# Performance work log

Measured on AMD Instinct MI355X. Metric: run time of the kernel, lower is better.

## Reference

```python
import jax, jax.numpy as jnp
import numpy as np

B, NQ = 4, 4096
HF, WF = 96, 96          # single-level feature map -> Nv = 9216
NV = HF * WF
E = 768                  # dim * num_frames = 192 * 4
NH, NP, NL = 8, 4, 1
HD = E // NH             # 96
EPS = 1e-6


def _layer_norm(x, w, b):
    m = jnp.mean(x, axis=-1, keepdims=True)
    v = jnp.var(x, axis=-1, keepdims=True)
    return (x - m) * jax.lax.rsqrt(v + EPS) * w + b


def _msda_core(value, shapes, loc, aw):
    # value: (B, Nv, H, D); loc: (B, Nq, H, L, P, 2) normalized in [0,1];
    # aw: (B, Nq, H, L, P). Bilinear sampling matching F.grid_sample
    # (align_corners=False, padding_mode='zeros'): pixel = loc * size - 0.5.
    Bn, Nv, H, D = value.shape
    Nq, P = loc.shape[1], loc.shape[4]
    out = jnp.zeros((Bn, H, Nq, D), value.dtype)
    start = 0
    for lvl in range(shapes.shape[0]):
        Hl, Wl = int(shapes[lvl, 0]), int(shapes[lvl, 1])
        v = value[:, start:start + Hl * Wl].transpose(0, 2, 1, 3)  # (B,H,S,D)
        start += Hl * Wl
        x = loc[:, :, :, lvl, :, 0] * Wl - 0.5  # (B,Nq,H,P)
        y = loc[:, :, :, lvl, :, 1] * Hl - 0.5
        x0, y0 = jnp.floor(x), jnp.floor(y)
        sampled = jnp.zeros((Bn, H, Nq, P, D), value.dtype)
        for dx in (0, 1):
            for dy in (0, 1):
                xi, yi = x0 + dx, y0 + dy
                w = (1.0 - jnp.abs(x - xi)) * (1.0 - jnp.abs(y - yi))
                valid = (xi >= 0) & (xi <= Wl - 1) & (yi >= 0) & (yi <= Hl - 1)
                idx = (jnp.clip(yi, 0, Hl - 1) * Wl
                       + jnp.clip(xi, 0, Wl - 1)).astype(jnp.int32)
                idx = idx.transpose(0, 2, 1, 3).reshape(Bn, H, Nq * P)
                g = jnp.take_along_axis(v, idx[..., None], axis=2)
                g = g.reshape(Bn, H, Nq, P, D)
                wz = jnp.where(valid, w, 0.0).transpose(0, 2, 1, 3)[..., None]
                sampled = sampled + g * wz
        awl = aw[:, :, :, lvl].transpose(0, 2, 1, 3)[..., None]  # (B,H,Nq,P,1)
        out = out + jnp.sum(sampled * awl, axis=3)
    return out.transpose(0, 2, 1, 3).reshape(Bn, Nq, H * D)


def setup_inputs():
    key = jax.random.key(0)
    ks = jax.random.split(key, 12)
    s = 0.02
    return {
        "query": jax.random.normal(ks[0], (B, NQ, E), jnp.float32),
        "reference_points": jax.random.uniform(ks[1], (B, NQ, NL, 2), jnp.float32),
        "feat": jax.random.normal(ks[2], (B, NV, E), jnp.float32),
        "spatial_shapes": jnp.array([[HF, WF]], jnp.int32),
        "level_start_index": jnp.zeros((NL,), jnp.int32),
        "ln_q_w": jnp.ones((E,), jnp.float32),
        "ln_q_b": jnp.zeros((E,), jnp.float32),
        "ln_f_w": jnp.ones((E,), jnp.float32),
        "ln_f_b": jnp.zeros((E,), jnp.float32),
        "W_value": jax.random.normal(ks[3], (E, E), jnp.float32) * s,
        "b_value": jnp.zeros((E,), jnp.float32),
        "W_off": jax.random.normal(ks[4], (E, NH * NL * NP * 2), jnp.float32) * s,
        "b_off": jax.random.normal(ks[5], (NH * NL * NP * 2,), jnp.float32) * s,
        "W_attn": jax.random.normal(ks[6], (E, NH * NL * NP), jnp.float32) * s,
        "b_attn": jnp.zeros((NH * NL * NP,), jnp.float32),
        "W_out": jax.random.normal(ks[7], (E, E), jnp.float32) * s,
        "b_out": jnp.zeros((E,), jnp.float32),
        "gamma": jax.random.normal(ks[8], (E,), jnp.float32) * s,
    }


def reference(query, reference_points, feat, spatial_shapes, level_start_index,
              ln_q_w, ln_q_b, ln_f_w, ln_f_b, W_value, b_value, W_off, b_off,
              W_attn, b_attn, W_out, b_out, gamma):
    shapes = np.asarray(spatial_shapes)  # static level shapes
    Bn, Nq, _ = query.shape
    Nv = feat.shape[1]
    q = _layer_norm(query, ln_q_w, ln_q_b)
    f = _layer_norm(feat, ln_f_w, ln_f_b)
    value = (f @ W_value + b_value).reshape(Bn, Nv, NH, HD)
    offsets = (q @ W_off + b_off).reshape(Bn, Nq, NH, NL, NP, 2)
    aw = jax.nn.softmax((q @ W_attn + b_attn).reshape(Bn, Nq, NH, NL * NP), -1)
    aw = aw.reshape(Bn, Nq, NH, NL, NP)
    # offset_normalizer = [W_l, H_l] per level
    norm = jnp.stack([jnp.asarray(shapes[:, 1], jnp.float32),
                      jnp.asarray(shapes[:, 0], jnp.float32)], axis=-1)  # (L,2)
    loc = (reference_points[:, :, None, :, None, :]
           + offsets / norm[None, None, None, :, None, :])
    out = _msda_core(value, shapes, loc, aw)
    out = out @ W_out + b_out
    attn = q + out  # mmcv MSDeformAttn adds identity (dropout=eval no-op)
    return query + gamma * attn
```

## Files before the change

kernel.cpp:

```cpp
#include <hip/hip_runtime.h>

#define BB     4
#define NQS    4096
#define NVS    9216
#define E_DIM  768
#define NHEAD  8
#define NPTS   4
#define HDIM   96
#define HFEAT  96
#define WFEAT  96
#define MQR    16384

typedef __attribute__((ext_vector_type(8))) short  s8v;
typedef __attribute__((ext_vector_type(4))) short  s4v;
typedef __attribute__((ext_vector_type(4))) float  f4v;

__device__ __forceinline__ unsigned short f2bf(float x) {
    unsigned int u = __builtin_bit_cast(unsigned int, x);
    unsigned int r = (u + 0x7fffu + ((u >> 16) & 1u)) >> 16;
    return (unsigned short)r;
}
__device__ __forceinline__ float bf2f(unsigned short s) {
    unsigned int u = ((unsigned int)s) << 16;
    return __builtin_bit_cast(float, u);
}
__device__ __forceinline__ float bf2f_s(short s) {
    return bf2f((unsigned short)s);
}

#define GLD16(gp, lp) \
    __builtin_amdgcn_global_load_lds( \
        (__attribute__((address_space(1))) void*)(gp), \
        (__attribute__((address_space(3))) void*)(lp), 16, 0, 0)

__global__ __launch_bounds__(256) void ln_fused_kernel(
    const float* __restrict__ q, const float* __restrict__ f,
    const float* __restrict__ qw, const float* __restrict__ qb,
    const float* __restrict__ fw, const float* __restrict__ fb,
    unsigned short* __restrict__ qout, unsigned short* __restrict__ fout,
    float* __restrict__ stats) {
    const int wv = threadIdx.x >> 6, lane = threadIdx.x & 63;
    const int row = blockIdx.x * 4 + wv;
    const bool isq = row < MQR;
    const float* x = isq ? (q + (size_t)row * E_DIM)
                         : (f + (size_t)(row - MQR) * E_DIM);
    const float4 v0 = ((const float4*)x)[lane];
    const float4 v1 = ((const float4*)x)[lane + 64];
    const float4 v2 = ((const float4*)x)[lane + 128];
    float s1 = v0.x + v0.y + v0.z + v0.w + v1.x + v1.y + v1.z + v1.w
             + v2.x + v2.y + v2.z + v2.w;
    float s2 = v0.x * v0.x + v0.y * v0.y + v0.z * v0.z + v0.w * v0.w
             + v1.x * v1.x + v1.y * v1.y + v1.z * v1.z + v1.w * v1.w
             + v2.x * v2.x + v2.y * v2.y + v2.z * v2.z + v2.w * v2.w;
    #pragma unroll
    for (int o = 32; o > 0; o >>= 1) {
        s1 += __shfl_down(s1, o, 64);
        s2 += __shfl_down(s2, o, 64);
    }
    const float mean = __shfl(s1, 0, 64) * (1.0f / E_DIM);
    const float m2   = __shfl(s2, 0, 64) * (1.0f / E_DIM);
    const float rstd = rsqrtf(m2 - mean * mean + 1e-6f);
    if (isq && lane == 0) { stats[row * 2] = mean; stats[row * 2 + 1] = rstd; }

    const float* w = isq ? qw : fw;
    const float* b = isq ? qb : fb;
    unsigned short* o = isq ? (qout + (size_t)row * E_DIM)
                            : (fout + (size_t)(row - MQR) * E_DIM);
    const float4 vv[3] = {v0, v1, v2};
    #pragma unroll
    for (int c = 0; c < 3; c++) {
        const float4 w4 = ((const float4*)w)[lane + c * 64];
        const float4 b4 = ((const float4*)b)[lane + c * 64];
        s4v ov;
        ov[0] = (short)f2bf((vv[c].x - mean) * rstd * w4.x + b4.x);
        ov[1] = (short)f2bf((vv[c].y - mean) * rstd * w4.y + b4.y);
        ov[2] = (short)f2bf((vv[c].z - mean) * rstd * w4.z + b4.z);
        ov[3] = (short)f2bf((vv[c].w - mean) * rstd * w4.w + b4.w);
        ((s4v*)o)[lane + c * 64] = ov;
    }
}

__global__ void transpose_cast2_kernel(const float* __restrict__ W0, const float* __restrict__ W1,
                                       unsigned short* __restrict__ T0, unsigned short* __restrict__ T1) {
    __shared__ float tile[32][33];
    const float* W = blockIdx.z ? W1 : W0;
    unsigned short* Wt = blockIdx.z ? T1 : T0;
    const int bi = blockIdx.y * 32, bj = blockIdx.x * 32;
    const int t = threadIdx.x;
    const int r = t >> 5, c = t & 31;
    #pragma unroll
    for (int i = 0; i < 4; i++)
        tile[r + i * 8][c] = W[(size_t)(bi + r + i * 8) * E_DIM + bj + c];
    __syncthreads();
    #pragma unroll
    for (int i = 0; i < 4; i++)
        Wt[(size_t)(bj + r + i * 8) * E_DIM + bi + c] = f2bf(tile[c][r + i * 8]);
}

__global__ void build_wqc_kernel(const float* __restrict__ W_off, const float* __restrict__ W_attn,
                                 const float* __restrict__ b_off, const float* __restrict__ b_attn,
                                 unsigned short* __restrict__ Wt, float* __restrict__ bcat) {
    const int idx = blockIdx.x * 256 + threadIdx.x;
    const int rrow = idx / E_DIM, k = idx % E_DIM;
    float v = 0.f;
    if (rrow < 64) v = W_off[(size_t)k * 64 + rrow];
    else if (rrow < 96) v = W_attn[(size_t)k * 32 + (rrow - 64)];
    Wt[idx] = f2bf(v);
    if (idx < 128) {
        float b = 0.f;
        if (idx < 64) b = b_off[idx];
        else if (idx < 96) b = b_attn[idx - 64];
        bcat[idx] = b;
    }
}

template <int EPI>
__global__ __launch_bounds__(256, 3) void mfma_gemm128(
    const unsigned short* __restrict__ A, const unsigned short* __restrict__ Bt,
    const float* __restrict__ bias, void* __restrict__ C, int ldC,
    const float* __restrict__ query, const float* __restrict__ qstats,
    const float* __restrict__ lnw, const float* __restrict__ lnb,
    const float* __restrict__ gamma) {
    __shared__ unsigned short As[128 * 64];
    __shared__ unsigned short Bs[128 * 64];

    constexpr int K = E_DIM;
    const int tid = threadIdx.x;
    const int wave = tid >> 6;
    const int lane = tid & 63;
    const int quad = lane >> 4;
    const int l16 = lane & 15;

    const int nwg = gridDim.x * gridDim.y;
    const int flat = blockIdx.y * gridDim.x + blockIdx.x;
    const int cpx = nwg >> 3;
    const int swz = (flat & 7) * cpx + (flat >> 3);
    const int bx = swz % gridDim.x;
    const int by = swz / gridDim.x;
    const int bm = by * 128;
    const int bn = bx * 128;
    const int wrow = wave >> 1, wcol = wave & 1;

    const unsigned short* arow[4];
    const unsigned short* brow[4];
    unsigned short* aldst[4];
    unsigned short* bldst[4];
    #pragma unroll
    for (int i = 0; i < 4; i++) {
        const int chunk = wave * 4 + i;
        const int s = chunk >> 1, r = (chunk & 1) * 64 + lane;
        arow[i] = A + (size_t)(bm + r) * K + s * 8;
        brow[i] = Bt + (size_t)(bn + r) * K + s * 8;
        aldst[i] = As + chunk * 512;
        bldst[i] = Bs + chunk * 512;
    }

    f4v acc[4][4] = {};

    for (int k0 = 0; k0 < K; k0 += 64) {
        #pragma unroll
        for (int i = 0; i < 4; i++)
            GLD16(arow[i] + k0, aldst[i]);
        #pragma unroll
        for (int i = 0; i < 4; i++)
            GLD16(brow[i] + k0, bldst[i]);

        __syncthreads();

        #pragma unroll
        for (int c = 0; c < 2; c++) {
            s8v af[4], bf[4];
            #pragma unroll
            for (int ti = 0; ti < 4; ti++)
                af[ti] = *(const s8v*)(As + ((size_t)((c * 4 + quad) * 128 + wrow * 64 + ti * 16 + l16)) * 8);
            #pragma unroll
            for (int tj = 0; tj < 4; tj++)
                bf[tj] = *(const s8v*)(Bs + ((size_t)((c * 4 + quad) * 128 + wcol * 64 + tj * 16 + l16)) * 8);
            #pragma unroll
            for (int ti = 0; ti < 4; ti++)
                #pragma unroll
                for (int tj = 0; tj < 4; tj++)
                    acc[ti][tj] = __builtin_amdgcn_mfma_f32_16x16x32_bf16(af[ti], bf[tj], acc[ti][tj], 0, 0, 0);
        }
        __syncthreads();
    }

    #pragma unroll
    for (int ti = 0; ti < 4; ti++) {
        const int gm_base = bm + wrow * 64 + ti * 16 + quad * 4;
        #pragma unroll
        for (int tj = 0; tj < 4; tj++) {
            const int gn = bn + wcol * 64 + tj * 16 + l16;
            const float bv = bias[gn];
            #pragma unroll
            for (int r = 0; r < 4; r++) {
                const int gm = gm_base + r;
                const float v = acc[ti][tj][r] + bv;
                if (EPI == 1) {
                    ((float*)C)[(size_t)gm * ldC + gn] = v;
                } else {
                    const size_t idx = (size_t)gm * ldC + gn;
                    const float qv = query[idx];
                    const float qln = (qv - qstats[gm * 2]) * qstats[gm * 2 + 1] * lnw[gn] + lnb[gn];
                    ((float*)C)[idx] = qv + gamma[gn] * (qln + v);
                }
            }
        }
    }
}

template <int G>
__device__ __forceinline__ void tigroup(const unsigned short* as_, const s8v (&bfr)[2][4],
                                        f4v (&acc)[8][4], int quad, int l16, int wrow) {
    s8v af[2][2];
    #pragma unroll
    for (int c = 0; c < 2; c++)
        #pragma unroll
        for (int m = 0; m < 2; m++)
            af[c][m] = *(const s8v*)(as_ + ((size_t)((c * 4 + quad) * 256 + wrow * 128 + (G * 2 + m) * 16 + l16)) * 8);
    #pragma unroll
    for (int c = 0; c < 2; c++)
        #pragma unroll
        for (int m = 0; m < 2; m++)
            #pragma unroll
            for (int n = 0; n < 4; n++)
                acc[G * 2 + m][n] = __builtin_amdgcn_mfma_f32_16x16x32_bf16(
                    af[c][m], bfr[c][n], acc[G * 2 + m][n], 0, 0, 0);
}

__global__ __launch_bounds__(512, 2) void mfma_gemm256(
    const unsigned short* __restrict__ A, const unsigned short* __restrict__ Bt,
    const float* __restrict__ bias, unsigned short* __restrict__ C) {
    __shared__ unsigned short As[2][256 * 64];
    __shared__ unsigned short Bs[2][256 * 64];

    constexpr int K = E_DIM;
    constexpr int NT = K / 64;
    const int tid = threadIdx.x;
    const int wave = tid >> 6;
    const int lane = tid & 63;
    const int quad = lane >> 4;
    const int l16 = lane & 15;

    const int nwg = gridDim.x * gridDim.y;
    const int flat = blockIdx.y * gridDim.x + blockIdx.x;
    const int cpx = nwg >> 3;
    const int swz = (flat & 7) * cpx + (flat >> 3);
    const int bx = swz % gridDim.x;
    const int by = swz / gridDim.x;
    const int bm = by * 256;
    const int bn = bx * 256;
    const int wrow = wave >> 2;
    const int wcol = wave & 3;

    const unsigned short* gsrc[4][2];
    int ldst[4][2];
    #pragma unroll
    for (int h = 0; h < 4; h++) {
        #pragma unroll
        for (int i = 0; i < 2; i++) {
            const int ch = wave * 2 + i;
            const int s = ch >> 1, rsub = ch & 1;
            const int rw = (h & 1) * 128 + rsub * 64 + lane;
            const unsigned short* base = (h < 2) ? (A + (size_t)(bm + rw) * K)
                                                 : (Bt + (size_t)(bn + rw) * K);
            gsrc[h][i] = base + s * 8;
            ldst[h][i] = (s * 256 + rw) * 8;
        }
    }

    #define STAGE256(h, kt, buf) do { \
        unsigned short* lb_ = ((h) < 2 ? &As[(buf)][0] : &Bs[(buf)][0]); \
        GLD16(gsrc[h][0] + (size_t)(kt) * 64, lb_ + ldst[h][0]); \
        GLD16(gsrc[h][1] + (size_t)(kt) * 64, lb_ + ldst[h][1]); \
    } while (0)

    f4v acc[8][4] = {};

    #pragma unroll
    for (int h = 0; h < 4; h++) STAGE256(h, 0, 0);

    int cur = 0;
    for (int t = 0; t < NT; ++t) {
        const unsigned short* as_ = &As[cur][0];
        const unsigned short* bs_ = &Bs[cur][0];
        const int nb = cur ^ 1;
        const bool pf = (t + 1 < NT);

        if (pf) {
            STAGE256(0, t + 1, nb);
            asm volatile("s_waitcnt vmcnt(2)" ::: "memory");
        } else {
            asm volatile("s_waitcnt vmcnt(0)" ::: "memory");
        }
        __builtin_amdgcn_s_barrier();
        __builtin_amdgcn_sched_barrier(0);

        s8v bfr[2][4];
        #pragma unroll
        for (int c = 0; c < 2; c++)
            #pragma unroll
            for (int n = 0; n < 4; n++)
                bfr[c][n] = *(const s8v*)(bs_ + ((size_t)((c * 4 + quad) * 256 + wcol * 64 + n * 16 + l16)) * 8);

        __builtin_amdgcn_s_setprio(1);
        tigroup<0>(as_, bfr, acc, quad, l16, wrow);
        __builtin_amdgcn_s_setprio(0);

        if (pf) STAGE256(1, t + 1, nb);
        __builtin_amdgcn_s_setprio(1);
        tigroup<1>(as_, bfr, acc, quad, l16, wrow);
        __builtin_amdgcn_s_setprio(0);

        if (pf) STAGE256(2, t + 1, nb);
        __builtin_amdgcn_s_setprio(1);
        tigroup<2>(as_, bfr, acc, quad, l16, wrow);
        __builtin_amdgcn_s_setprio(0);

        if (pf) STAGE256(3, t + 1, nb);
        s8v af3[2][2];
        #pragma unroll
        for (int c = 0; c < 2; c++)
            #pragma unroll
            for (int m = 0; m < 2; m++)
                af3[c][m] = *(const s8v*)(as_ + ((size_t)((c * 4 + quad) * 256 + wrow * 128 + (6 + m) * 16 + l16)) * 8);
        asm volatile("s_waitcnt lgkmcnt(0)" ::: "memory");
        __builtin_amdgcn_sched_barrier(0);
        __builtin_amdgcn_s_barrier();
        __builtin_amdgcn_sched_barrier(0);
        __builtin_amdgcn_s_setprio(1);
        #pragma unroll
        for (int c = 0; c < 2; c++)
            #pragma unroll
            for (int m = 0; m < 2; m++)
                #pragma unroll
                for (int n = 0; n < 4; n++)
                    acc[6 + m][n] = __builtin_amdgcn_mfma_f32_16x16x32_bf16(
                        af3[c][m], bfr[c][n], acc[6 + m][n], 0, 0, 0);
        __builtin_amdgcn_s_setprio(0);

        cur ^= 1;
    }
    #undef STAGE256

    #pragma unroll
    for (int ti = 0; ti < 8; ti++) {
        const int gm_base = bm + wrow * 128 + ti * 16 + quad * 4;
        #pragma unroll
        for (int tj = 0; tj < 4; tj++) {
            const int gn = bn + wcol * 64 + tj * 16 + l16;
            const float bv = bias[gn];
            const int hh = gn / HDIM, dd = gn - hh * HDIM;
            #pragma unroll
            for (int r = 0; r < 4; r++) {
                const int gm = gm_base + r;
                const float v = acc[ti][tj][r] + bv;
                const int b = gm / NVS, s = gm - b * NVS;
                const size_t vidx = (((size_t)b * NHEAD + hh) * NVS + s) * HDIM + dd;
                C[vidx] = f2bf(v);
            }
        }
    }
}

__global__ __launch_bounds__(384) void msda_kernel(
    const unsigned short* __restrict__ value,
    const float* __restrict__ oa,
    const float* __restrict__ refp,
    unsigned short* __restrict__ out) {
    const int h = blockIdx.x;
    const int row0 = blockIdx.y * 32;
    const int t = threadIdx.x;

    __shared__ float x_s[128], y_s[128], aw_s[128];
    if (t < 128) {
        const int r = t >> 2, p = t & 3;
        const int row = row0 + r;
        const float* oar = oa + (size_t)row * 128;
        float a = oar[64 + h * 4 + p];
        float mx = fmaxf(a, __shfl_xor(a, 1, 64));
        mx = fmaxf(mx, __shfl_xor(mx, 2, 64));
        float e = __expf(a - mx);
        float sden = e + __shfl_xor(e, 1, 64);
        sden += __shfl_xor(sden, 2, 64);
        aw_s[t] = e / sden;
        const float rx = refp[(size_t)row * 2 + 0] * WFEAT - 0.5f;
        const float ry = refp[(size_t)row * 2 + 1] * HFEAT - 0.5f;
        x_s[t] = rx + oar[h * 8 + p * 2 + 0];
        y_s[t] = ry + oar[h * 8 + p * 2 + 1];
    }
    __syncthreads();

    const int r = t / 12;
    const int j = t - r * 12;
    const int row = row0 + r;
    const int b = row >> 12;
    const unsigned short* vb = value + ((size_t)(b * NHEAD + h) * NVS) * HDIM + j * 8;

    float acc[8] = {};
    #pragma unroll
    for (int p = 0; p < 4; p++) {
        const float x = x_s[r * 4 + p];
        const float y = y_s[r * 4 + p];
        const float aw = aw_s[r * 4 + p];
        const float x0f = floorf(x), y0f = floorf(y);
        const float fx = x - x0f, fy = y - y0f;
        const int ix0 = (int)x0f, iy0 = (int)y0f;
        const int ix1 = ix0 + 1, iy1 = iy0 + 1;
        const float wx0 = (ix0 >= 0 && ix0 < WFEAT) ? (1.f - fx) : 0.f;
        const float wx1 = (ix1 >= 0 && ix1 < WFEAT) ? fx : 0.f;
        const float wy0 = (iy0 >= 0 && iy0 < HFEAT) ? (1.f - fy) : 0.f;
        const float wy1 = (iy1 >= 0 && iy1 < HFEAT) ? fy : 0.f;
        const int cx0 = min(max(ix0, 0), WFEAT - 1);
        const int cx1 = min(max(ix1, 0), WFEAT - 1);
        const int cy0 = min(max(iy0, 0), HFEAT - 1);
        const int cy1 = min(max(iy1, 0), HFEAT - 1);
        const float w00 = aw * wy0 * wx0, w01 = aw * wy0 * wx1;
        const float w10 = aw * wy1 * wx0, w11 = aw * wy1 * wx1;
        const s8v v00 = *(const s8v*)(vb + (size_t)(cy0 * WFEAT + cx0) * HDIM);
        const s8v v01 = *(const s8v*)(vb + (size_t)(cy0 * WFEAT + cx1) * HDIM);
        const s8v v10 = *(const s8v*)(vb + (size_t)(cy1 * WFEAT + cx0) * HDIM);
        const s8v v11 = *(const s8v*)(vb + (size_t)(cy1 * WFEAT + cx1) * HDIM);
        #pragma unroll
        for (int k = 0; k < 8; k++) {
            acc[k] += w00 * bf2f_s(v00[k]) + w01 * bf2f_s(v01[k])
                    + w10 * bf2f_s(v10[k]) + w11 * bf2f_s(v11[k]);
        }
    }

    s8v o;
    #pragma unroll
    for (int k = 0; k < 8; k++) o[k] = (short)f2bf(acc[k]);
    *(s8v*)(out + (size_t)row * E_DIM + h * HDIM + j * 8) = o;
}

extern "C" void kernel_launch(void* const* d_in, const int* in_sizes, int n_in,
                              void* d_out, int out_size, void* d_ws, size_t ws_size,
                              hipStream_t stream) {
    (void)in_sizes; (void)n_in; (void)out_size; (void)ws_size;

    const float* query  = (const float*)d_in[0];
    const float* refp   = (const float*)d_in[1];
    const float* feat   = (const float*)d_in[2];
    const float* ln_q_w = (const float*)d_in[5];
    const float* ln_q_b = (const float*)d_in[6];
    const float* ln_f_w = (const float*)d_in[7];
    const float* ln_f_b = (const float*)d_in[8];
    const float* W_val  = (const float*)d_in[9];
    const float* b_val  = (const float*)d_in[10];
    const float* W_off  = (const float*)d_in[11];
    const float* b_off  = (const float*)d_in[12];
    const float* W_attn = (const float*)d_in[13];
    const float* b_attn = (const float*)d_in[14];
    const float* W_out  = (const float*)d_in[15];
    const float* b_out  = (const float*)d_in[16];
    const float* gamma  = (const float*)d_in[17];
    float* out = (float*)d_out;

    const int MQ = BB * NQS;
    const int MV = BB * NVS;

    char* ws = (char*)d_ws;
    float*          q_stats = (float*)(ws + 0);
    unsigned short* qbf     = (unsigned short*)(ws + 131072);
    unsigned short* fbf     = (unsigned short*)(ws + 25296896);
    unsigned short* val_bf  = (unsigned short*)(ws + 81920000);
    unsigned short* msda_bf = (unsigned short*)(ws + 138543104);
    float*          offattn = (float*)(ws + 163708928);
    unsigned short* Wv_t    = (unsigned short*)(ws + 172097536);
    unsigned short* Wo_t    = (unsigned short*)(ws + 173277184);
    unsigned short* Wqc_t   = (unsigned short*)(ws + 174456832);
    float*          bcat    = (float*)(ws + 174653440);

    ln_fused_kernel<<<(MQ + MV) / 4, 256, 0, stream>>>(
        query, feat, ln_q_w, ln_q_b, ln_f_w, ln_f_b, qbf, fbf, q_stats);

    transpose_cast2_kernel<<<dim3(24, 24, 2), 256, 0, stream>>>(W_val, W_out, Wv_t, Wo_t);
    build_wqc_kernel<<<384, 256, 0, stream>>>(W_off, W_attn, b_off, b_attn, Wqc_t, bcat);

    mfma_gemm256<<<dim3(E_DIM / 256, MV / 256), 512, 0, stream>>>(
        fbf, Wv_t, b_val, val_bf);

    mfma_gemm128<1><<<dim3(1, MQ / 128), 256, 0, stream>>>(
        qbf, Wqc_t, bcat, offattn, 128, nullptr, nullptr, nullptr, nullptr, nullptr);

    msda_kernel<<<dim3(NHEAD, MQ / 32), 384, 0, stream>>>(val_bf, offattn, refp, msda_bf);

    mfma_gemm128<2><<<dim3(E_DIM / 128, MQ / 128), 256, 0, stream>>>(
        msda_bf, Wo_t, b_out, out, E_DIM, query, q_stats, ln_q_w, ln_q_b, gamma);
}
```

Baseline: 470.2 us.

## Merge prep kernels into one launch and fold query projection into value GEMM grid

Merges the LayerNorm, weight transpose/cast and Wqc build kernels into one prep kernel dispatched by block index. The offset/attention projection GEMM now runs as extra blocks appended to the value-projection GEMM grid, using a simple single-buffered MFMA loop. This removes three kernel launches and lets the small query GEMM fill idle CUs alongside the 432 value tiles. The cost is a larger combined kernel whose register and LDS footprint is set by the heavier branch, which may limit occupancy for the small-GEMM blocks.

```diff
diff --git a/kernel.cpp b/kernel.cpp
--- a/kernel.cpp
+++ b/kernel.cpp
@@ -10,6 +10,9 @@
 #define HFEAT  96
 #define WFEAT  96
 #define MQR    16384
+#define NLNB   13312
+#define NTRB   1152
+#define NVALB  432
 
 typedef __attribute__((ext_vector_type(8))) short  s8v;
 typedef __attribute__((ext_vector_type(4))) short  s4v;
@@ -33,91 +36,93 @@
         (__attribute__((address_space(1))) void*)(gp), \
         (__attribute__((address_space(3))) void*)(lp), 16, 0, 0)
 
-__global__ __launch_bounds__(256) void ln_fused_kernel(
+__global__ __launch_bounds__(256) void prep_kernel(
     const float* __restrict__ q, const float* __restrict__ f,
     const float* __restrict__ qw, const float* __restrict__ qb,
     const float* __restrict__ fw, const float* __restrict__ fb,
     unsigned short* __restrict__ qout, unsigned short* __restrict__ fout,
-    float* __restrict__ stats) {
-    const int wv = threadIdx.x >> 6, lane = threadIdx.x & 63;
-    const int row = blockIdx.x * 4 + wv;
-    const bool isq = row < MQR;
-    const float* x = isq ? (q + (size_t)row * E_DIM)
-                         : (f + (size_t)(row - MQR) * E_DIM);
-    const float4 v0 = ((const float4*)x)[lane];
-    const float4 v1 = ((const float4*)x)[lane + 64];
-    const float4 v2 = ((const float4*)x)[lane + 128];
-    float s1 = v0.x + v0.y + v0.z + v0.w + v1.x + v1.y + v1.z + v1.w
-             + v2.x + v2.y + v2.z + v2.w;
-    float s2 = v0.x * v0.x + v0.y * v0.y + v0.z * v0.z + v0.w * v0.w
-             + v1.x * v1.x + v1.y * v1.y + v1.z * v1.z + v1.w * v1.w
-             + v2.x * v2.x + v2.y * v2.y + v2.z * v2.z + v2.w * v2.w;
-    #pragma unroll
-    for (int o = 32; o > 0; o >>= 1) {
-        s1 += __shfl_down(s1, o, 64);
-        s2 += __shfl_down(s2, o, 64);
-    }
-    const float mean = __shfl(s1, 0, 64) * (1.0f / E_DIM);
-    const float m2   = __shfl(s2, 0, 64) * (1.0f / E_DIM);
-    const float rstd = rsqrtf(m2 - mean * mean + 1e-6f);
-    if (isq && lane == 0) { stats[row * 2] = mean; stats[row * 2 + 1] = rstd; }
-
-    const float* w = isq ? qw : fw;
-    const float* b = isq ? qb : fb;
-    unsigned short* o = isq ? (qout + (size_t)row * E_DIM)
-                            : (fout + (size_t)(row - MQR) * E_DIM);
-    const float4 vv[3] = {v0, v1, v2};
-    #pragma unroll
-    for (int c = 0; c < 3; c++) {
-        const float4 w4 = ((const float4*)w)[lane + c * 64];
-        const float4 b4 = ((const float4*)b)[lane + c * 64];
-        s4v ov;
-        ov[0] = (short)f2bf((vv[c].x - mean) * rstd * w4.x + b4.x);
-        ov[1] = (short)f2bf((vv[c].y - mean) * rstd * w4.y + b4.y);
-        ov[2] = (short)f2bf((vv[c].z - mean) * rstd * w4.z + b4.z);
-        ov[3] = (short)f2bf((vv[c].w - mean) * rstd * w4.w + b4.w);
-        ((s4v*)o)[lane + c * 64] = ov;
-    }
-}
-
-__global__ void transpose_cast2_kernel(const float* __restrict__ W0, const float* __restrict__ W1,
-                                       unsigned short* __restrict__ T0, unsigned short* __restrict__ T1) {
+    float* __restrict__ stats,
+    const float* __restrict__ W0, const float* __restrict__ W1,
+    unsigned short* __restrict__ T0, unsigned short* __restrict__ T1,
+    const float* __restrict__ W_off, const float* __restrict__ W_attn,
+    const float* __restrict__ b_off, const float* __restrict__ b_attn,
+    unsigned short* __restrict__ Wqc, float* __restrict__ bcat) {
     __shared__ float tile[32][33];
-    const float* W = blockIdx.z ? W1 : W0;
-    unsigned short* Wt = blockIdx.z ? T1 : T0;
-    const int bi = blockIdx.y * 32, bj = blockIdx.x * 32;
-    const int t = threadIdx.x;
-    const int r = t >> 5, c = t & 31;
-    #pragma unroll
-    for (int i = 0; i < 4; i++)
-        tile[r + i * 8][c] = W[(size_t)(bi + r + i * 8) * E_DIM + bj + c];
-    __syncthreads();
-    #pragma unroll
-    for (int i = 0; i < 4; i++)
-        Wt[(size_t)(bj + r + i * 8) * E_DIM + bi + c] = f2bf(tile[c][r + i * 8]);
-}
-
-__global__ void build_wqc_kernel(const float* __restrict__ W_off, const float* __restrict__ W_attn,
-                                 const float* __restrict__ b_off, const float* __restrict__ b_attn,
-                                 unsigned short* __restrict__ Wt, float* __restrict__ bcat) {
-    const int idx = blockIdx.x * 256 + threadIdx.x;
-    const int rrow = idx / E_DIM, k = idx % E_DIM;
-    float v = 0.f;
-    if (rrow < 64) v = W_off[(size_t)k * 64 + rrow];
-    else if (rrow < 96) v = W_attn[(size_t)k * 32 + (rrow - 64)];
-    Wt[idx] = f2bf(v);
-    if (idx < 128) {
-        float b = 0.f;
-        if (idx < 64) b = b_off[idx];
-        else if (idx < 96) b = b_attn[idx - 64];
-        bcat[idx] = b;
-    }
-}
-
-template <int EPI>
+    const int bid = blockIdx.x;
+
+    if (bid < NLNB) {
+        const int wv = threadIdx.x >> 6, lane = threadIdx.x & 63;
+        const int row = bid * 4 + wv;
+        const bool isq = row < MQR;
+        const float* x = isq ? (q + (size_t)row * E_DIM)
+                             : (f + (size_t)(row - MQR) * E_DIM);
+        const float4 v0 = ((const float4*)x)[lane];
+        const float4 v1 = ((const float4*)x)[lane + 64];
+        const float4 v2 = ((const float4*)x)[lane + 128];
+        float s1 = v0.x + v0.y + v0.z + v0.w + v1.x + v1.y + v1.z + v1.w
+                 + v2.x + v2.y + v2.z + v2.w;
+        float s2 = v0.x * v0.x + v0.y * v0.y + v0.z * v0.z + v0.w * v0.w
+                 + v1.x * v1.x + v1.y * v1.y + v1.z * v1.z + v1.w * v1.w
+                 + v2.x * v2.x + v2.y * v2.y + v2.z * v2.z + v2.w * v2.w;
+        #pragma unroll
+        for (int o = 32; o > 0; o >>= 1) {
+            s1 += __shfl_down(s1, o, 64);
+            s2 += __shfl_down(s2, o, 64);
+        }
+        const float mean = __shfl(s1, 0, 64) * (1.0f / E_DIM);
+        const float m2   = __shfl(s2, 0, 64) * (1.0f / E_DIM);
+        const float rstd = rsqrtf(m2 - mean * mean + 1e-6f);
+        if (isq && lane == 0) { stats[row * 2] = mean; stats[row * 2 + 1] = rstd; }
+        const float* w = isq ? qw : fw;
+        const float* b = isq ? qb : fb;
+        unsigned short* o = isq ? (qout + (size_t)row * E_DIM)
+                                : (fout + (size_t)(row - MQR) * E_DIM);
+        const float4 vv[3] = {v0, v1, v2};
+        #pragma unroll
+        for (int c = 0; c < 3; c++) {
+            const float4 w4 = ((const float4*)w)[lane + c * 64];
+            const float4 b4 = ((const float4*)b)[lane + c * 64];
+            s4v ov;
+            ov[0] = (short)f2bf((vv[c].x - mean) * rstd * w4.x + b4.x);
+            ov[1] = (short)f2bf((vv[c].y - mean) * rstd * w4.y + b4.y);
+            ov[2] = (short)f2bf((vv[c].z - mean) * rstd * w4.z + b4.z);
+            ov[3] = (short)f2bf((vv[c].w - mean) * rstd * w4.w + b4.w);
+            ((s4v*)o)[lane + c * 64] = ov;
+        }
+    } else if (bid < NLNB + NTRB) {
+        const int idx = bid - NLNB;
+        const int z = idx / 576, r2 = idx - z * 576;
+        const float* W = z ? W1 : W0;
+        unsigned short* Wt = z ? T1 : T0;
+        const int bi = (r2 / 24) * 32, bj = (r2 % 24) * 32;
+        const int t = threadIdx.x;
+        const int r = t >> 5, c = t & 31;
+        #pragma unroll
+        for (int i = 0; i < 4; i++)
+            tile[r + i * 8][c] = W[(size_t)(bi + r + i * 8) * E_DIM + bj + c];
+        __syncthreads();
+        #pragma unroll
+        for (int i = 0; i < 4; i++)
+            Wt[(size_t)(bj + r + i * 8) * E_DIM + bi + c] = f2bf(tile[c][r + i * 8]);
+    } else {
+        const int idx = (bid - NLNB - NTRB) * 256 + threadIdx.x;
+        const int rrow = idx / E_DIM, k = idx % E_DIM;
+        float v = 0.f;
+        if (rrow < 64) v = W_off[(size_t)k * 64 + rrow];
+        else if (rrow < 96) v = W_attn[(size_t)k * 32 + (rrow - 64)];
+        Wqc[idx] = f2bf(v);
+        if (idx < 128) {
+            float b = 0.f;
+            if (idx < 64) b = b_off[idx];
+            else if (idx < 96) b = b_attn[idx - 64];
+            bcat[idx] = b;
+        }
+    }
+}
+
 __global__ __launch_bounds__(256, 3) void mfma_gemm128(
     const unsigned short* __restrict__ A, const unsigned short* __restrict__ Bt,
-    const float* __restrict__ bias, void* __restrict__ C, int ldC,
+    const float* __restrict__ bias, float* __restrict__ C, int ldC,
     const float* __restrict__ query, const float* __restrict__ qstats,
     const float* __restrict__ lnw, const float* __restrict__ lnb,
     const float* __restrict__ gamma) {
@@ -196,14 +201,10 @@
             for (int r = 0; r < 4; r++) {
                 const int gm = gm_base + r;
                 const float v = acc[ti][tj][r] + bv;
-                if (EPI == 1) {
-                    ((float*)C)[(size_t)gm * ldC + gn] = v;
-                } else {
-                    const size_t idx = (size_t)gm * ldC + gn;
-                    const float qv = query[idx];
-                    const float qln = (qv - qstats[gm * 2]) * qstats[gm * 2 + 1] * lnw[gn] + lnb[gn];
-                    ((float*)C)[idx] = qv + gamma[gn] * (qln + v);
-                }
+                const size_t idx = (size_t)gm * ldC + gn;
+                const float qv = query[idx];
+                const float qln = (qv - qstats[gm * 2]) * qstats[gm * 2 + 1] * lnw[gn] + lnb[gn];
+                C[idx] = qv + gamma[gn] * (qln + v);
             }
         }
     }
@@ -230,7 +231,9 @@
 
 __global__ __launch_bounds__(512, 2) void mfma_gemm256(
     const unsigned short* __restrict__ A, const unsigned short* __restrict__ Bt,
-    const float* __restrict__ bias, unsigned short* __restrict__ C) {
+    const float* __restrict__ bias, unsigned short* __restrict__ C,
+    const unsigned short* __restrict__ Aq, const unsigned short* __restrict__ Wqc,
+    const float* __restrict__ bcat, float* __restrict__ offattn) {
     __shared__ unsigned short As[2][256 * 64];
     __shared__ unsigned short Bs[2][256 * 64];
 
@@ -242,122 +245,182 @@
     const int quad = lane >> 4;
     const int l16 = lane & 15;
 
-    const int nwg = gridDim.x * gridDim.y;
-    const int flat = blockIdx.y * gridDim.x + blockIdx.x;
-    const int cpx = nwg >> 3;
-    const int swz = (flat & 7) * cpx + (flat >> 3);
-    const int bx = swz % gridDim.x;
-    const int by = swz / gridDim.x;
-    const int bm = by * 256;
-    const int bn = bx * 256;
-    const int wrow = wave >> 2;
-    const int wcol = wave & 3;
-
-    const unsigned short* gsrc[4][2];
-    int ldst[4][2];
-    #pragma unroll
-    for (int h = 0; h < 4; h++) {
+    if (blockIdx.x < NVALB) {
+        const int flat = blockIdx.x;
+        const int cpx = NVALB >> 3;
+        const int swz = (flat & 7) * cpx + (flat >> 3);
+        const int bx = swz % 3;
+        const int by = swz / 3;
+        const int bm = by * 256;
+        const int bn = bx * 256;
+        const int wrow = wave >> 2;
+        const int wcol = wave & 3;
+
+        const unsigned short* gsrc[4][2];
+        int ldst[4][2];
+        #pragma unroll
+        for (int h = 0; h < 4; h++) {
+            #pragma unroll
+            for (int i = 0; i < 2; i++) {
+                const int ch = wave * 2 + i;
+                const int s = ch >> 1, rsub = ch & 1;
+                const int rw = (h & 1) * 128 + rsub * 64 + lane;
+                const unsigned short* base = (h < 2) ? (A + (size_t)(bm + rw) * K)
+                                                     : (Bt + (size_t)(bn + rw) * K);
+                gsrc[h][i] = base + s * 8;
+                ldst[h][i] = (s * 256 + rw) * 8;
+            }
+        }
+
+        #define STAGE256(h, kt, buf) do { \
+            unsigned short* lb_ = ((h) < 2 ? &As[(buf)][0] : &Bs[(buf)][0]); \
+            GLD16(gsrc[h][0] + (size_t)(kt) * 64, lb_ + ldst[h][0]); \
+            GLD16(gsrc[h][1] + (size_t)(kt) * 64, lb_ + ldst[h][1]); \
+        } while (0)
+
+        f4v acc[8][4] = {};
+
+        #pragma unroll
+        for (int h = 0; h < 4; h++) STAGE256(h, 0, 0);
+
+        int cur = 0;
+        for (int t = 0; t < NT; ++t) {
+            const unsigned short* as_ = &As[cur][0];
+            const unsigned short* bs_ = &Bs[cur][0];
+            const int nb = cur ^ 1;
+            const bool pf = (t + 1 < NT);
+
+            if (pf) {
+                STAGE256(0, t + 1, nb);
+                asm volatile("s_waitcnt vmcnt(2)" ::: "memory");
+            } else {
+                asm volatile("s_waitcnt vmcnt(0)" ::: "memory");
+            }
+            __builtin_amdgcn_s_barrier();
+            __builtin_amdgcn_sched_barrier(0);
+
+            s8v bfr[2][4];
+            #pragma unroll
+            for (int c = 0; c < 2; c++)
+                #pragma unroll
+                for (int n = 0; n < 4; n++)
+                    bfr[c][n] = *(const s8v*)(bs_ + ((size_t)((c * 4 + quad) * 256 + wcol * 64 + n * 16 + l16)) * 8);
+
+            __builtin_amdgcn_s_setprio(1);
+            tigroup<0>(as_, bfr, acc, quad, l16, wrow);
+            __builtin_amdgcn_s_setprio(0);
+
+            if (pf) STAGE256(1, t + 1, nb);
+            __builtin_amdgcn_s_setprio(1);
+            tigroup<1>(as_, bfr, acc, quad, l16, wrow);
+            __builtin_amdgcn_s_setprio(0);
+
+            if (pf) STAGE256(2, t + 1, nb);
+            __builtin_amdgcn_s_setprio(1);
+            tigroup<2>(as_, bfr, acc, quad, l16, wrow);
+            __builtin_amdgcn_s_setprio(0);
+
+            if (pf) STAGE256(3, t + 1, nb);
+            s8v af3[2][2];
+            #pragma unroll
+            for (int c = 0; c < 2; c++)
+                #pragma unroll
+                for (int m = 0; m < 2; m++)
+                    af3[c][m] = *(const s8v*)(as_ + ((size_t)((c * 4 + quad) * 256 + wrow * 128 + (6 + m) * 16 + l16)) * 8);
+            asm volatile("s_waitcnt lgkmcnt(0)" ::: "memory");
+            __builtin_amdgcn_sched_barrier(0);
+            __builtin_amdgcn_s_barrier();
+            __builtin_amdgcn_sched_barrier(0);
+            __builtin_amdgcn_s_setprio(1);
+            #pragma unroll
+            for (int c = 0; c < 2; c++)
+                #pragma unroll
+                for (int m = 0; m < 2; m++)
+                    #pragma unroll
+                    for (int n = 0; n < 4; n++)
+                        acc[6 + m][n] = __builtin_amdgcn_mfma_f32_16x16x32_bf16(
+                            af3[c][m], bfr[c][n], acc[6 + m][n], 0, 0, 0);
+            __builtin_amdgcn_s_setprio(0);
+
+            cur ^= 1;
+        }
+        #undef STAGE256
+
+        #pragma unroll
+        for (int ti = 0; ti < 8; ti++) {
+            const int gm_base = bm + wrow * 128 + ti * 16 + quad * 4;
+            #pragma unroll
+            for (int tj = 0; tj < 4; tj++) {
+                const int gn = bn + wcol * 64 + tj * 16 + l16;
+                const float bv = bias[gn];
+                const int hh = gn / HDIM, dd = gn - hh * HDIM;
+                #pragma unroll
+                for (int r = 0; r < 4; r++) {
+                    const int gm = gm_base + r;
+                    const float v = acc[ti][tj][r] + bv;
+                    const int b = gm / NVS, s = gm - b * NVS;
+                    const size_t vidx = (((size_t)b * NHEAD + hh) * NVS + s) * HDIM + dd;
+                    C[vidx] = f2bf(v);
+                }
+            }
+        }
+    } else {
+        const int bm = (blockIdx.x - NVALB) * 128;
+        const int wrow = wave >> 2;
+        const int wcol = wave & 3;
+        unsigned short* As0 = &As[0][0];
+        unsigned short* Bs0 = &Bs[0][0];
+
+        const unsigned short* arow[2];
+        const unsigned short* brow[2];
+        int loff[2];
         #pragma unroll
         for (int i = 0; i < 2; i++) {
             const int ch = wave * 2 + i;
-            const int s = ch >> 1, rsub = ch & 1;
-            const int rw = (h & 1) * 128 + rsub * 64 + lane;
-            const unsigned short* base = (h < 2) ? (A + (size_t)(bm + rw) * K)
-                                                 : (Bt + (size_t)(bn + rw) * K);
-            gsrc[h][i] = base + s * 8;
-            ldst[h][i] = (s * 256 + rw) * 8;
-        }
-    }
-
-    #define STAGE256(h, kt, buf) do { \
-        unsigned short* lb_ = ((h) < 2 ? &As[(buf)][0] : &Bs[(buf)][0]); \
-        GLD16(gsrc[h][0] + (size_t)(kt) * 64, lb_ + ldst[h][0]); \
-        GLD16(gsrc[h][1] + (size_t)(kt) * 64, lb_ + ldst[h][1]); \
-    } while (0)
-
-    f4v acc[8][4] = {};
-
-    #pragma unroll
-    for (int h = 0; h < 4; h++) STAGE256(h, 0, 0);
-
-    int cur = 0;
-    for (int t = 0; t < NT; ++t) {
-        const unsigned short* as_ = &As[cur][0];
-        const unsigned short* bs_ = &Bs[cur][0];
-        const int nb = cur ^ 1;
-        const bool pf = (t + 1 < NT);
-
-        if (pf) {
-            STAGE256(0, t + 1, nb);
-            asm volatile("s_waitcnt vmcnt(2)" ::: "memory");
-        } else {
-            asm volatile("s_waitcnt vmcnt(0)" ::: "memory");
-        }
-        __builtin_amdgcn_s_barrier();
-        __builtin_amdgcn_sched_barrier(0);
-
-        s8v bfr[2][4];
-        #pragma unroll
-        for (int c = 0; c < 2; c++)
-            #pragma unroll
-            for (int n = 0; n < 4; n++)
-                bfr[c][n] = *(const s8v*)(bs_ + ((size_t)((c * 4 + quad) * 256 + wcol * 64 + n * 16 + l16)) * 8);
-
-        __builtin_amdgcn_s_setprio(1);
-        tigroup<0>(as_, bfr, acc, quad, l16, wrow);
-        __builtin_amdgcn_s_setprio(0);
-
-        if (pf) STAGE256(1, t + 1, nb);
-        __builtin_amdgcn_s_setprio(1);
-        tigroup<1>(as_, bfr, acc, quad, l16, wrow);
-        __builtin_amdgcn_s_setprio(0);
-
-        if (pf) STAGE256(2, t + 1, nb);
-        __builtin_amdgcn_s_setprio(1);
-        tigroup<2>(as_, bfr, acc, quad, l16, wrow);
-        __builtin_amdgcn_s_setprio(0);
-
-        if (pf) STAGE256(3, t + 1, nb);
-        s8v af3[2][2];
-        #pragma unroll
-        for (int c = 0; c < 2; c++)
-            #pragma unroll
-            for (int m = 0; m < 2; m++)
-                af3[c][m] = *(const s8v*)(as_ + ((size_t)((c * 4 + quad) * 256 + wrow * 128 + (6 + m) * 16 + l16)) * 8);
-        asm volatile("s_waitcnt lgkmcnt(0)" ::: "memory");
-        __builtin_amdgcn_sched_barrier(0);
-        __builtin_amdgcn_s_barrier();
-        __builtin_amdgcn_sched_barrier(0);
-        __builtin_amdgcn_s_setprio(1);
-        #pragma unroll
-        for (int c = 0; c < 2; c++)
-            #pragma unroll
-            for (int m = 0; m < 2; m++)
-                #pragma unroll
-                for (int n = 0; n < 4; n++)
-                    acc[6 + m][n] = __builtin_amdgcn_mfma_f32_16x16x32_bf16(
-                        af3[c][m], bfr[c][n], acc[6 + m][n], 0, 0, 0);
-        __builtin_amdgcn_s_setprio(0);
-
-        cur ^= 1;
-    }
-    #undef STAGE256
-
-    #pragma unroll
-    for (int ti = 0; ti < 8; ti++) {
-        const int gm_base = bm + wrow * 128 + ti * 16 + quad * 4;
-        #pragma unroll
-        for (int tj = 0; tj < 4; tj++) {
-            const int gn = bn + wcol * 64 + tj * 16 + l16;
-            const float bv = bias[gn];
-            const int hh = gn / HDIM, dd = gn - hh * HDIM;
-            #pragma unroll
-            for (int r = 0; r < 4; r++) {
-                const int gm = gm_base + r;
-                const float v = acc[ti][tj][r] + bv;
-                const int b = gm / NVS, s = gm - b * NVS;
-                const size_t vidx = (((size_t)b * NHEAD + hh) * NVS + s) * HDIM + dd;
-                C[vidx] = f2bf(v);
+            const int s = ch >> 1, r = (ch & 1) * 64 + lane;
+            arow[i] = Aq + (size_t)(bm + r) * K + s * 8;
+            brow[i] = Wqc + (size_t)r * K + s * 8;
+            loff[i] = (s * 128 + r) * 8;
+        }
+
+        f4v accq[4][2] = {};
+
+        for (int k0 = 0; k0 < K; k0 += 64) {
+            #pragma unroll
+            for (int i = 0; i < 2; i++) GLD16(arow[i] + k0, As0 + loff[i]);
+            #pragma unroll
+            for (int i = 0; i < 2; i++) GLD16(brow[i] + k0, Bs0 + loff[i]);
+
+            __syncthreads();
+
+            #pragma unroll
+            for (int c = 0; c < 2; c++) {
+                s8v af[4], bf[2];
+                #pragma unroll
+                for (int m = 0; m < 4; m++)
+                    af[m] = *(const s8v*)(As0 + ((size_t)((c * 4 + quad) * 128 + wrow * 64 + m * 16 + l16)) * 8);
+                #pragma unroll
+                for (int n = 0; n < 2; n++)
+                    bf[n] = *(const s8v*)(Bs0 + ((size_t)((c * 4 + quad) * 128 + wcol * 32 + n * 16 + l16)) * 8);
+                #pragma unroll
+                for (int m = 0; m < 4; m++)
+                    #pragma unroll
+                    for (int n = 0; n < 2; n++)
+                        accq[m][n] = __builtin_amdgcn_mfma_f32_16x16x32_bf16(af[m], bf[n], accq[m][n], 0, 0, 0);
+            }
+            __syncthreads();
+        }
+
+        #pragma unroll
+        for (int m = 0; m < 4; m++) {
+            const int gm_base = bm + wrow * 64 + m * 16 + quad * 4;
+            #pragma unroll
+            for (int n = 0; n < 2; n++) {
+                const int gn = wcol * 32 + n * 16 + l16;
+                const float bv = bcat[gn];
+                #pragma unroll
+                for (int r = 0; r < 4; r++)
+                    offattn[(size_t)(gm_base + r) * 128 + gn] = accq[m][n][r] + bv;
             }
         }
     }
@@ -472,20 +535,15 @@
     unsigned short* Wqc_t   = (unsigned short*)(ws + 174456832);
     float*          bcat    = (float*)(ws + 174653440);
 
-    ln_fused_kernel<<<(MQ + MV) / 4, 256, 0, stream>>>(
-        query, feat, ln_q_w, ln_q_b, ln_f_w, ln_f_b, qbf, fbf, q_stats);
-
-    transpose_cast2_kernel<<<dim3(24, 24, 2), 256, 0, stream>>>(W_val, W_out, Wv_t, Wo_t);
-    build_wqc_kernel<<<384, 256, 0, stream>>>(W_off, W_attn, b_off, b_attn, Wqc_t, bcat);
-
-    mfma_gemm256<<<dim3(E_DIM / 256, MV / 256), 512, 0, stream>>>(
-        fbf, Wv_t, b_val, val_bf);
-
-    mfma_gemm128<1><<<dim3(1, MQ / 128), 256, 0, stream>>>(
-        qbf, Wqc_t, bcat, offattn, 128, nullptr, nullptr, nullptr, nullptr, nullptr);
+    prep_kernel<<<NLNB + NTRB + 384, 256, 0, stream>>>(
+        query, feat, ln_q_w, ln_q_b, ln_f_w, ln_f_b, qbf, fbf, q_stats,
+        W_val, W_out, Wv_t, Wo_t, W_off, W_attn, b_off, b_attn, Wqc_t, bcat);
+
+    mfma_gemm256<<<NVALB + 128, 512, 0, stream>>>(
+        fbf, Wv_t, b_val, val_bf, qbf, Wqc_t, bcat, offattn);
 
     msda_kernel<<<dim3(NHEAD, MQ / 32), 384, 0, stream>>>(val_bf, offattn, refp, msda_bf);
 
-    mfma_gemm128<2><<<dim3(E_DIM / 128, MQ / 128), 256, 0, stream>>>(
+    mfma_gemm128<<<dim3(E_DIM / 128, MQ / 128), 256, 0, stream>>>(
         msda_bf, Wo_t, b_out, out, E_DIM, query, q_stats, ln_q_w, ln_q_b, gamma);
 }
```

Result: faster. 442.9 us (-5.8%).
